# Kernel tuning notes

Hardware: AMD Instinct MI355X
Metric: run time of the kernel (lower is better)

The kernel has to match this reference:

```python
import jax, jax.numpy as jnp
import numpy as np

SINUSOIDAL_EMBEDDING_BASE = 10000.0
WEIGHT_INIT_SCALE = 0.02
B = 524288
X_DIM = 128
T_EMB_DIM = 32
HIDDEN = 64
INPUT_DIM = 1 + X_DIM + T_EMB_DIM  # 161


def timestep_embedding(t, dim):
    # t: [B] int or float -> [B, dim] sinusoidal embedding
    half = dim // 2
    freqs = jnp.exp(-jnp.log(jnp.float32(SINUSOIDAL_EMBEDDING_BASE)) * jnp.arange(half, dtype=jnp.float32) / half)
    args = t[:, None].astype(jnp.float32) * freqs[None, :]
    emb = jnp.concatenate([jnp.sin(args), jnp.cos(args)], axis=1)
    if dim % 2 == 1:
        emb = jnp.concatenate([emb, jnp.zeros((t.shape[0], 1), dtype=emb.dtype)], axis=1)
    return emb


def setup_inputs() -> dict:
    key = jax.random.key(0)
    k1, k2, k3, k4, k5 = jax.random.split(key, 5)
    y_t = jax.random.normal(k1, (B, 1), dtype=jnp.float32)
    t = jax.random.randint(k2, (B,), 0, 1000, dtype=jnp.int32)
    x = jax.random.normal(k3, (B, X_DIM), dtype=jnp.float32)
    fc1_weight = jax.random.normal(k4, (HIDDEN, INPUT_DIM), dtype=jnp.float32) * WEIGHT_INIT_SCALE
    fc1_bias = jnp.zeros((HIDDEN,), dtype=jnp.float32)
    fc2_weight = jax.random.normal(k5, (1, HIDDEN), dtype=jnp.float32) * WEIGHT_INIT_SCALE
    fc2_bias = jnp.zeros((1,), dtype=jnp.float32)
    return {"y_t": y_t, "t": t, "x": x,
            "fc1_weight": fc1_weight, "fc1_bias": fc1_bias,
            "fc2_weight": fc2_weight, "fc2_bias": fc2_bias}


def reference(y_t, t, x, fc1_weight, fc1_bias, fc2_weight, fc2_bias):
    te = timestep_embedding(t, T_EMB_DIM)              # [B, t_emb_dim]
    inp = jnp.concatenate([y_t, x, te], axis=1)        # [B, input_dim]
    # The original's per-unit loop (sum(inp * W[i]) + b[i]) is exactly a matmul.
    h = jax.nn.relu(inp @ fc1_weight.T + fc1_bias)     # [B, hidden]
    out = h @ fc2_weight.T + fc2_bias                  # [B, 1]
    return out
```

## Files before the change

kernel.cpp:

```cpp
#include <hip/hip_runtime.h>
#include <hip/hip_bf16.h>


typedef __bf16 bf16x8 __attribute__((ext_vector_type(8)));
typedef float  f32x4  __attribute__((ext_vector_type(4)));

#define NROWS   524288
#define KSTEPS  6
#define NTILES  4

static __device__ inline unsigned short f2bf(float x) {
    union { float f; unsigned u; } v; v.f = x;
    unsigned r = v.u + 0x7FFFu + ((v.u >> 16) & 1u);
    return (unsigned short)(r >> 16);
}

static __device__ inline bf16x8 cvt8(float4 a, float4 b) {
    uint4 r;
    r.x = (unsigned)f2bf(a.x) | ((unsigned)f2bf(a.y) << 16);
    r.y = (unsigned)f2bf(a.z) | ((unsigned)f2bf(a.w) << 16);
    r.z = (unsigned)f2bf(b.x) | ((unsigned)f2bf(b.y) << 16);
    r.w = (unsigned)f2bf(b.z) | ((unsigned)f2bf(b.w) << 16);
    return __builtin_bit_cast(bf16x8, r);
}

static __device__ inline void gload_lds16(const void* g, void* l) {
    __builtin_amdgcn_global_load_lds(
        (const __attribute__((address_space(1))) unsigned int*)g,
        (__attribute__((address_space(3))) unsigned int*)l, 16, 0, 0);
}

__global__ void setup_tables(const float* __restrict__ w1, const float* __restrict__ b1,
                             unsigned short* __restrict__ wf, unsigned short* __restrict__ tab) {
    int tid = blockIdx.x * blockDim.x + threadIdx.x;
    if (tid < 1536) {
        int l  = tid & 63;
        int fs = tid >> 6;
        int n  = fs / 6;
        int s  = fs % 6;
        int col = 16 * n + (l & 15);
        int g   = l >> 4;
        unsigned short vals[8] __attribute__((aligned(16)));
        #pragma unroll
        for (int j = 0; j < 8; ++j) {
            int k = 32 * s + 8 * g + j;
            float v;
            if      (k < 160)  v = w1[col * 161 + k + 1];
            else if (k == 160) v = w1[col * 161 + 0];
            else if (k == 161) v = b1[col];
            else               v = 0.0f;
            vals[j] = f2bf(v);
        }
        ((uint4*)wf)[tid] = *(const uint4*)vals;
    }
    if (tid < 16000) {
        int t = tid >> 4;
        int j = tid & 15;
        float freq = expf((-9.2103403719761836f * (float)j) * 0.0625f);
        float a    = (float)t * freq;
        tab[t * 32 + j]      = f2bf(sinf(a));
        tab[t * 32 + 16 + j] = f2bf(cosf(a));
    }
}

__global__ __launch_bounds__(256, 4) void mlp_kernel(
    const float* __restrict__ y_t, const int* __restrict__ t, const float* __restrict__ x,
    const float* __restrict__ w2, const float* __restrict__ b2p,
    const unsigned short* __restrict__ wfrag, const unsigned short* __restrict__ tetab,
    float* __restrict__ out)
{
    __shared__ __align__(16) float ldsx[64 * 128];
    const int tid = threadIdx.x;
    const int l   = tid & 63;
    const int wv  = tid >> 6;
    const int r   = l & 15;
    const int g   = l >> 4;
    const long long trow0 = (long long)blockIdx.x * 64 + wv * 16;
    const long long arow  = trow0 + r;

    int   tval = t[arow];
    float yv   = y_t[arow];

    float w2f[4];
    #pragma unroll
    for (int n = 0; n < NTILES; ++n) w2f[n] = w2[16 * n + r];
    const float b2 = b2p[0];

    {
        const int rr = l >> 5;
        const int c  = l & 31;
        #pragma unroll
        for (int i = 0; i < 8; ++i) {
            const int rowrel = 2 * i + rr;
            const int csrc   = c ^ (rowrel & 7);
            const float* src = x + (trow0 + rowrel) * 128 + csrc * 4;
            gload_lds16(src, (void*)(ldsx + wv * 2048 + i * 256));
        }
    }
    asm volatile("s_waitcnt vmcnt(0)" ::: "memory");

    bf16x8 af[KSTEPS];
    {
        const float4* lx = (const float4*)ldsx;
        const int base = wv * 512 + r * 32;
        const int sw   = r & 7;
        #pragma unroll
        for (int s = 0; s < 4; ++s) {
            int c0 = 8 * s + 2 * g;
            float4 a = lx[base + ((c0    ) ^ sw)];
            float4 b = lx[base + ((c0 + 1) ^ sw)];
            af[s] = cvt8(a, b);
        }
    }
    {
        tval = tval < 0 ? 0 : (tval > 999 ? 999 : tval);
        af[4] = *(const bf16x8*)(tetab + tval * 32 + 8 * g);
    }
    {
        uint4 u = make_uint4(0u, 0u, 0u, 0u);
        if (g == 0) u.x = (unsigned)f2bf(yv) | (0x3F80u << 16);
        af[5] = __builtin_bit_cast(bf16x8, u);
    }

    const bf16x8* __restrict__ wfv = (const bf16x8*)wfrag;
    f32x4 acc[NTILES];
    #pragma unroll
    for (int n = 0; n < NTILES; ++n) acc[n] = (f32x4){0.f, 0.f, 0.f, 0.f};
    #pragma unroll
    for (int n = 0; n < NTILES; ++n)
        #pragma unroll
        for (int s = 0; s < KSTEPS; ++s)
            acc[n] = __builtin_amdgcn_mfma_f32_16x16x32_bf16(
                af[s], wfv[(n * 6 + s) * 64 + l], acc[n], 0, 0, 0);

    float4 p;
    float* pp = &p.x;
    #pragma unroll
    for (int v = 0; v < 4; ++v) {
        float pv = 0.f;
        #pragma unroll
        for (int n = 0; n < NTILES; ++n) pv += w2f[n] * fmaxf(acc[n][v], 0.f);
        pv += __shfl_xor(pv, 1);
        pv += __shfl_xor(pv, 2);
        pv += __shfl_xor(pv, 4);
        pv += __shfl_xor(pv, 8);
        pp[v] = pv + b2;
    }
    if (r == 0) {
        *(float4*)(out + trow0 + 4 * g) = p;
    }
}

extern "C" void kernel_launch(void* const* d_in, const int* in_sizes, int n_in,
                              void* d_out, int out_size, void* d_ws, size_t ws_size,
                              hipStream_t stream) {
    const float* y_t = (const float*)d_in[0];
    const int*   t   = (const int*)  d_in[1];
    const float* x   = (const float*)d_in[2];
    const float* w1  = (const float*)d_in[3];
    const float* b1  = (const float*)d_in[4];
    const float* w2  = (const float*)d_in[5];
    const float* b2  = (const float*)d_in[6];

    unsigned short* wfrag = (unsigned short*)d_ws;
    unsigned short* tetab = wfrag + 12288;

    setup_tables<<<64, 256, 0, stream>>>(w1, b1, wfrag, tetab);
    mlp_kernel<<<NROWS / 64, 256, 0, stream>>>(y_t, t, x, w2, b2, wfrag, tetab, (float*)d_out);
}
```

Baseline: 385.8 us.

## Make MLP kernel persistent with register double-buffered x prefetch

Replaces the one-tile-per-block launch with a fixed grid of 512 persistent blocks. Each wave loops over 16 row tiles and prefetches the next tile's x, t and y_t into registers while it computes the current tile. The LDS staging through global_load_lds is removed, and x is now read directly into registers with per-lane 32-byte strided accesses. The intent is to overlap loads with MFMA work and cut block launch overhead. In exchange it lowers occupancy (launch bounds drop to 2 blocks) and may reduce the number of memory requests in flight per CU.

Measured after the change: 377.7 us. -2.1%, faster.

```diff
diff --git a/kernel.cpp b/kernel.cpp
--- a/kernel.cpp
+++ b/kernel.cpp
@@ -8,6 +8,8 @@
 #define NROWS   524288
 #define KSTEPS  6
 #define NTILES  4
+#define GRID    512
+#define ITERS   16
 
 static __device__ inline unsigned short f2bf(float x) {
     union { float f; unsigned u; } v; v.f = x;
@@ -22,12 +24,6 @@
     r.z = (unsigned)f2bf(b.x) | ((unsigned)f2bf(b.y) << 16);
     r.w = (unsigned)f2bf(b.z) | ((unsigned)f2bf(b.w) << 16);
     return __builtin_bit_cast(bf16x8, r);
-}
-
-static __device__ inline void gload_lds16(const void* g, void* l) {
-    __builtin_amdgcn_global_load_lds(
-        (const __attribute__((address_space(1))) unsigned int*)g,
-        (__attribute__((address_space(3))) unsigned int*)l, 16, 0, 0);
 }
 
 __global__ void setup_tables(const float* __restrict__ w1, const float* __restrict__ b1,
@@ -63,91 +59,106 @@
     }
 }
 
-__global__ __launch_bounds__(256, 4) void mlp_kernel(
+static __device__ inline int clamp_t(int tv) {
+    return tv < 0 ? 0 : (tv > 999 ? 999 : tv);
+}
+
+__global__ __launch_bounds__(256, 2) void mlp_kernel(
     const float* __restrict__ y_t, const int* __restrict__ t, const float* __restrict__ x,
     const float* __restrict__ w2, const float* __restrict__ b2p,
     const unsigned short* __restrict__ wfrag, const unsigned short* __restrict__ tetab,
     float* __restrict__ out)
 {
-    __shared__ __align__(16) float ldsx[64 * 128];
     const int tid = threadIdx.x;
     const int l   = tid & 63;
     const int wv  = tid >> 6;
     const int r   = l & 15;
     const int g   = l >> 4;
-    const long long trow0 = (long long)blockIdx.x * 64 + wv * 16;
-    const long long arow  = trow0 + r;
-
-    int   tval = t[arow];
-    float yv   = y_t[arow];
 
     float w2f[4];
     #pragma unroll
     for (int n = 0; n < NTILES; ++n) w2f[n] = w2[16 * n + r];
     const float b2 = b2p[0];
+    const bf16x8* __restrict__ wfv = (const bf16x8*)wfrag;
 
+    long long tile = (long long)blockIdx.x * 64 + wv;
+    long long row  = tile * 16 + r;
+
+    float4 cx[8];
     {
-        const int rr = l >> 5;
-        const int c  = l & 31;
+        const float4* xr = (const float4*)(x + row * 128);
         #pragma unroll
-        for (int i = 0; i < 8; ++i) {
-            const int rowrel = 2 * i + rr;
-            const int csrc   = c ^ (rowrel & 7);
-            const float* src = x + (trow0 + rowrel) * 128 + csrc * 4;
-            gload_lds16(src, (void*)(ldsx + wv * 2048 + i * 256));
+        for (int s = 0; s < 4; ++s) {
+            cx[2 * s]     = xr[8 * s + 2 * g];
+            cx[2 * s + 1] = xr[8 * s + 2 * g + 1];
         }
     }
-    asm volatile("s_waitcnt vmcnt(0)" ::: "memory");
+    int   t_cur = clamp_t(t[row]);
+    float y_cur = y_t[row];
 
-    bf16x8 af[KSTEPS];
-    {
-        const float4* lx = (const float4*)ldsx;
-        const int base = wv * 512 + r * 32;
-        const int sw   = r & 7;
+    #pragma unroll 1
+    for (int i = 0; i < ITERS; ++i) {
+        float4 nx[8];
+        int    t_nxt = 0;
+        float  y_nxt = 0.f;
+        const bool has_next = (i + 1 < ITERS);
+        if (has_next) {
+            const long long nrow = row + 64;
+            const float4* xr = (const float4*)(x + nrow * 128);
+            #pragma unroll
+            for (int s = 0; s < 4; ++s) {
+                nx[2 * s]     = xr[8 * s + 2 * g];
+                nx[2 * s + 1] = xr[8 * s + 2 * g + 1];
+            }
+            t_nxt = t[nrow];
+            y_nxt = y_t[nrow];
+        }
+
+        bf16x8 af[KSTEPS];
         #pragma unroll
-        for (int s = 0; s < 4; ++s) {
-            int c0 = 8 * s + 2 * g;
-            float4 a = lx[base + ((c0    ) ^ sw)];
-            float4 b = lx[base + ((c0 + 1) ^ sw)];
-            af[s] = cvt8(a, b);
+        for (int s = 0; s < 4; ++s) af[s] = cvt8(cx[2 * s], cx[2 * s + 1]);
+        af[4] = *(const bf16x8*)(tetab + t_cur * 32 + 8 * g);
+        {
+            uint4 u = make_uint4(0u, 0u, 0u, 0u);
+            if (g == 0) u.x = (unsigned)f2bf(y_cur) | (0x3F80u << 16);
+            af[5] = __builtin_bit_cast(bf16x8, u);
         }
-    }
-    {
-        tval = tval < 0 ? 0 : (tval > 999 ? 999 : tval);
-        af[4] = *(const bf16x8*)(tetab + tval * 32 + 8 * g);
-    }
-    {
-        uint4 u = make_uint4(0u, 0u, 0u, 0u);
-        if (g == 0) u.x = (unsigned)f2bf(yv) | (0x3F80u << 16);
-        af[5] = __builtin_bit_cast(bf16x8, u);
-    }
 
-    const bf16x8* __restrict__ wfv = (const bf16x8*)wfrag;
-    f32x4 acc[NTILES];
-    #pragma unroll
-    for (int n = 0; n < NTILES; ++n) acc[n] = (f32x4){0.f, 0.f, 0.f, 0.f};
-    #pragma unroll
-    for (int n = 0; n < NTILES; ++n)
+        f32x4 acc[NTILES];
         #pragma unroll
-        for (int s = 0; s < KSTEPS; ++s)
-            acc[n] = __builtin_amdgcn_mfma_f32_16x16x32_bf16(
-                af[s], wfv[(n * 6 + s) * 64 + l], acc[n], 0, 0, 0);
+        for (int n = 0; n < NTILES; ++n) acc[n] = (f32x4){0.f, 0.f, 0.f, 0.f};
+        #pragma unroll
+        for (int n = 0; n < NTILES; ++n)
+            #pragma unroll
+            for (int s = 0; s < KSTEPS; ++s)
+                acc[n] = __builtin_amdgcn_mfma_f32_16x16x32_bf16(
+                    af[s], wfv[(n * 6 + s) * 64 + l], acc[n], 0, 0, 0);
 
-    float4 p;
-    float* pp = &p.x;
-    #pragma unroll
-    for (int v = 0; v < 4; ++v) {
-        float pv = 0.f;
+        float4 p;
+        float* pp = &p.x;
         #pragma unroll
-        for (int n = 0; n < NTILES; ++n) pv += w2f[n] * fmaxf(acc[n][v], 0.f);
-        pv += __shfl_xor(pv, 1);
-        pv += __shfl_xor(pv, 2);
-        pv += __shfl_xor(pv, 4);
-        pv += __shfl_xor(pv, 8);
-        pp[v] = pv + b2;
-    }
-    if (r == 0) {
-        *(float4*)(out + trow0 + 4 * g) = p;
+        for (int v = 0; v < 4; ++v) {
+            float pv = 0.f;
+            #pragma unroll
+            for (int n = 0; n < NTILES; ++n) pv += w2f[n] * fmaxf(acc[n][v], 0.f);
+            pv += __shfl_xor(pv, 1);
+            pv += __shfl_xor(pv, 2);
+            pv += __shfl_xor(pv, 4);
+            pv += __shfl_xor(pv, 8);
+            pp[v] = pv + b2;
+        }
+        if (r == 0) {
+            *(float4*)(out + tile * 16 + 4 * g) = p;
+        }
+
+        if (has_next) {
+            #pragma unroll
+            for (int s = 0; s < 8; ++s) cx[s] = nx[s];
+            t_cur = clamp_t(t_nxt);
+            y_cur = y_nxt;
+        }
+        tile += 4;
+        row  += 64;
     }
 }
 
@@ -166,5 +177,5 @@
     unsigned short* tetab = wfrag + 12288;
 
     setup_tables<<<64, 256, 0, stream>>>(w1, b1, wfrag, tetab);
-    mlp_kernel<<<NROWS / 64, 256, 0, stream>>>(y_t, t, x, w2, b2, wfrag, tetab, (float*)d_out);
+    mlp_kernel<<<GRID, 256, 0, stream>>>(y_t, t, x, w2, b2, wfrag, tetab, (float*)d_out);
 }
```
